# Optimization experiments

Measured on AMD Instinct MI355X. Metric: run time of the kernel, lower is better.

The kernel has to match this reference:

```python
import jax, jax.numpy as jnp
import numpy as np

MARGIN = 0.5
B, C, P, N = 32768, 64, 16, 48  # problems, candidates/problem, max pos, max neg


def setup_inputs() -> dict:
    key = jax.random.key(0)
    k0, k1, k2, k3, k4 = jax.random.split(key, 5)
    return {
        "scores": jax.random.normal(k0, (B * C,), dtype=jnp.float32),
        "pos_indices": jax.random.randint(k1, (B, P), 0, C, dtype=jnp.int32),
        "neg_indices": jax.random.randint(k2, (B, N), 0, C, dtype=jnp.int32),
        "pos_counts": jax.random.randint(k3, (B,), 0, P + 1, dtype=jnp.int32),
        "neg_counts": jax.random.randint(k4, (B,), 0, N + 1, dtype=jnp.int32),
    }


def reference(scores, pos_indices, neg_indices, pos_counts, neg_counts):
    b, p = pos_indices.shape
    n = neg_indices.shape[1]
    c = scores.shape[0] // b
    # per-problem offsets into the flat score vector (uniform candidate_counts = c)
    offs = (jnp.arange(b, dtype=jnp.int32) * c)[:, None]
    pos = scores[offs + pos_indices]  # [B, P]
    neg = scores[offs + neg_indices]  # [B, N]
    # ragged validity masks (count == 0 reproduces the skip for empty lists)
    pos_mask = (jnp.arange(p, dtype=jnp.int32)[None, :] < pos_counts[:, None])
    neg_mask = (jnp.arange(n, dtype=jnp.int32)[None, :] < neg_counts[:, None])
    pair_mask = (pos_mask[:, :, None] & neg_mask[:, None, :]).astype(scores.dtype)  # [B,P,N]
    # relu(margin - pos + neg) over every pos x neg pair within each problem
    pair_loss = jax.nn.relu(MARGIN - pos[:, :, None] + neg[:, None, :])
    total = jnp.sum(pair_loss * pair_mask)
    count = jnp.sum(pair_mask)
    return jnp.where(count > 0, total / jnp.maximum(count, 1.0), jnp.array(0.0, scores.dtype))
```

## Files before the change

kernel.cpp:

```cpp
#include <hip/hip_runtime.h>


#define MARGIN 0.5f

constexpr int C = 64;
constexpr int P = 16;
constexpr int N = 48;
constexpr int BLOCK = 256;
constexpr int WAVES_PER_BLOCK = BLOCK / 64;
constexpr int PROBS_PER_WAVE = 4;
constexpr int PROBS_PER_BLOCK = WAVES_PER_BLOCK * PROBS_PER_WAVE;

__global__ __launch_bounds__(BLOCK) void mpcl_partial_kernel(
    const float* __restrict__ scores,
    const int*   __restrict__ pos_indices,
    const int*   __restrict__ neg_indices,
    const int*   __restrict__ pos_counts,
    const int*   __restrict__ neg_counts,
    float2*      __restrict__ partials,
    int B)
{
    const int lane = threadIdx.x & 63;
    const int wave = threadIdx.x >> 6;

    float tot = 0.0f;
    float cnt = 0.0f;

    const int b0 = (blockIdx.x * WAVES_PER_BLOCK + wave) * PROBS_PER_WAVE;

    for (int k = 0; k < PROBS_PER_WAVE; ++k) {
        const int b = b0 + k;
        if (b >= B) break;

        const int pc = pos_counts[b];
        const int nc = neg_counts[b];

        float myval  = 0.0f;
        float negval = -1e30f;
        if (lane >= 48) {
            const int idx = pos_indices[b * P + (lane - 48)];
            myval = scores[b * C + idx];
        } else if (lane < nc) {
            const int idx = neg_indices[b * N + lane];
            negval = scores[b * C + idx];
        }

        float s = 0.0f;
        for (int i = 0; i < pc; ++i) {
            const float pos_i = __shfl(myval, 48 + i);
            s += fmaxf(MARGIN - pos_i + negval, 0.0f);
        }
        tot += s;
        cnt += (float)(pc * nc);
    }

    #pragma unroll
    for (int off = 32; off; off >>= 1) tot += __shfl_xor(tot, off);

    __shared__ float2 lds[WAVES_PER_BLOCK];
    if (lane == 0) lds[wave] = make_float2(tot, cnt);
    __syncthreads();

    if (threadIdx.x == 0) {
        float2 acc = lds[0];
        #pragma unroll
        for (int w = 1; w < WAVES_PER_BLOCK; ++w) { acc.x += lds[w].x; acc.y += lds[w].y; }
        partials[blockIdx.x] = acc;
    }
}

__global__ __launch_bounds__(BLOCK) void mpcl_final_kernel(
    const float2* __restrict__ partials, int n, float* __restrict__ out)
{
    float tot = 0.0f, cnt = 0.0f;
    for (int i = threadIdx.x; i < n; i += BLOCK) {
        const float2 p = partials[i];
        tot += p.x;
        cnt += p.y;
    }
    #pragma unroll
    for (int off = 32; off; off >>= 1) {
        tot += __shfl_xor(tot, off);
        cnt += __shfl_xor(cnt, off);
    }

    __shared__ float2 lds[WAVES_PER_BLOCK];
    const int wave = threadIdx.x >> 6;
    const int lane = threadIdx.x & 63;
    if (lane == 0) lds[wave] = make_float2(tot, cnt);
    __syncthreads();

    if (threadIdx.x == 0) {
        float T = 0.0f, Cn = 0.0f;
        #pragma unroll
        for (int w = 0; w < WAVES_PER_BLOCK; ++w) { T += lds[w].x; Cn += lds[w].y; }
        out[0] = (Cn > 0.0f) ? (T / fmaxf(Cn, 1.0f)) : 0.0f;
    }
}

extern "C" void kernel_launch(void* const* d_in, const int* in_sizes, int n_in,
                              void* d_out, int out_size, void* d_ws, size_t ws_size,
                              hipStream_t stream) {
    const float* scores      = (const float*)d_in[0];
    const int*   pos_indices = (const int*)d_in[1];
    const int*   neg_indices = (const int*)d_in[2];
    const int*   pos_counts  = (const int*)d_in[3];
    const int*   neg_counts  = (const int*)d_in[4];
    float*       out         = (float*)d_out;

    const int B = in_sizes[3];
    const int grid = (B + PROBS_PER_BLOCK - 1) / PROBS_PER_BLOCK;

    float2* partials = (float2*)d_ws;

    mpcl_partial_kernel<<<grid, BLOCK, 0, stream>>>(
        scores, pos_indices, neg_indices, pos_counts, neg_counts, partials, B);
    mpcl_final_kernel<<<1, BLOCK, 0, stream>>>(partials, grid, out);
}
```

Before: 80.11 us.

## Load scores row coalesced and gather via shuffles, unroll fixed pos loop

Each wave now reads its problem's full 64-entry score row with one coalesced load and gathers pos/neg values with a cross-lane shuffle, replacing the dependent random global gather. The pos loop becomes a fixed 16-iteration unrolled loop with two accumulators, and invalid positives are masked with large sentinels, which removes the data-dependent trip count. Problems per wave rise from 4 to 8 and the problem loop is unrolled to give more independent loads in flight. The cost is always doing 16 iterations even when the pos count is small, plus higher register use.

```diff
diff --git a/kernel.cpp b/kernel.cpp
--- a/kernel.cpp
+++ b/kernel.cpp
@@ -8,7 +8,7 @@
 constexpr int N = 48;
 constexpr int BLOCK = 256;
 constexpr int WAVES_PER_BLOCK = BLOCK / 64;
-constexpr int PROBS_PER_WAVE = 4;
+constexpr int PROBS_PER_WAVE = 8;
 constexpr int PROBS_PER_BLOCK = WAVES_PER_BLOCK * PROBS_PER_WAVE;
 
 __global__ __launch_bounds__(BLOCK) void mpcl_partial_kernel(
@@ -28,29 +28,36 @@
 
     const int b0 = (blockIdx.x * WAVES_PER_BLOCK + wave) * PROBS_PER_WAVE;
 
+    #pragma unroll
     for (int k = 0; k < PROBS_PER_WAVE; ++k) {
         const int b = b0 + k;
-        if (b >= B) break;
+        const bool valid = (b < B);
 
-        const int pc = pos_counts[b];
-        const int nc = neg_counts[b];
-
-        float myval  = 0.0f;
-        float negval = -1e30f;
-        if (lane >= 48) {
-            const int idx = pos_indices[b * P + (lane - 48)];
-            myval = scores[b * C + idx];
-        } else if (lane < nc) {
-            const int idx = neg_indices[b * N + lane];
-            negval = scores[b * C + idx];
+        int   pc = 0, nc = 0;
+        float sc = 0.0f;
+        int   idx = 0;
+        if (valid) {
+            pc  = pos_counts[b];
+            nc  = neg_counts[b];
+            sc  = scores[b * C + lane];
+            idx = (lane < N) ? neg_indices[b * N + lane]
+                             : pos_indices[b * P + (lane - N)];
         }
 
-        float s = 0.0f;
-        for (int i = 0; i < pc; ++i) {
-            const float pos_i = __shfl(myval, 48 + i);
-            s += fmaxf(MARGIN - pos_i + negval, 0.0f);
+        const float g = __shfl(sc, idx);
+
+        const float myval  = (lane >= N) ? (((lane - N) < pc) ? g : 1e30f) : 0.0f;
+        const float negval = (lane <  N) ? ((lane < nc) ? g : -1e30f) : -1e30f;
+
+        float s0 = 0.0f, s1 = 0.0f;
+        #pragma unroll
+        for (int i = 0; i < P; i += 2) {
+            const float p0 = __shfl(myval, N + i);
+            const float p1 = __shfl(myval, N + i + 1);
+            s0 += fmaxf(MARGIN - p0 + negval, 0.0f);
+            s1 += fmaxf(MARGIN - p1 + negval, 0.0f);
         }
-        tot += s;
+        tot += s0 + s1;
         cnt += (float)(pc * nc);
     }
 
```

Measured after the change: 81.89 us. 2.2% more time.
